# Performance work log

Measured on AMD Instinct MI355X. Metric: run time of the kernel, lower is better.

The kernel has to match this reference:

```python
import jax, jax.numpy as jnp
import numpy as np

DIM_IN = 1024
DIM_OUT = 1024


def setup_inputs() -> dict:
    key = jax.random.key(0)
    k1, k2, k3, k4 = jax.random.split(key, 4)
    X = jax.random.normal(k1, (4, 2048, DIM_IN), dtype=jnp.float32)
    s = 1.0 / np.sqrt(DIM_IN)
    Wq = jax.random.normal(k2, (DIM_IN, DIM_OUT), dtype=jnp.float32) * s
    Wk = jax.random.normal(k3, (DIM_IN, DIM_OUT), dtype=jnp.float32) * s
    Wv = jax.random.normal(k4, (DIM_IN, DIM_OUT), dtype=jnp.float32) * s
    return {"X": X, "Wq": Wq, "Wk": Wk, "Wv": Wv}


def reference(X, Wq, Wk, Wv):
    # X: [B, T, Din]; projections (qkv_bias=False)
    q = jnp.einsum('btd,de->bte', X, Wq)   # [B, T, Dout]
    k = jnp.einsum('btd,de->bte', X, Wk)
    v = jnp.einsum('btd,de->bte', X, Wv)
    T = X.shape[1]
    scores = jnp.einsum('bqe,bke->bqk', q, k)  # [B, T, T]
    causal = jnp.tril(jnp.ones((T, T), dtype=bool))  # mask upper triangle (future)
    scores = jnp.where(causal, scores, -jnp.inf)
    # scale=True: divide by sqrt(d); -inf stays -inf so order vs mask is irrelevant
    scores = scores / jnp.sqrt(jnp.asarray(k.shape[-1], dtype=scores.dtype))
    weights = jax.nn.softmax(scores, axis=-1)
    # dropout p=0.0 -> identity
    return jnp.einsum('bqk,bke->bqe', weights, v)
```

## Files before the change

kernel.cpp:

```cpp
#include <hip/hip_runtime.h>
#include <hip/hip_bf16.h>

typedef unsigned short u16;
typedef __bf16 bf16x8 __attribute__((ext_vector_type(8)));
typedef float f32x4 __attribute__((ext_vector_type(4)));
typedef unsigned short u16x8 __attribute__((ext_vector_type(8)));
typedef unsigned short u16x4 __attribute__((ext_vector_type(4)));

__device__ __forceinline__ float bf2f(u16 u) {
  unsigned int x = ((unsigned int)u) << 16;
  return __builtin_bit_cast(float, x);
}
__device__ __forceinline__ u16 f2bf(float f) {
  unsigned int x = __builtin_bit_cast(unsigned int, f);
  x = x + 0x7FFFu + ((x >> 16) & 1u);
  return (u16)(x >> 16);
}

__device__ __forceinline__ void gload_lds16(const u16* g, u16* l) {
  __builtin_amdgcn_global_load_lds(
      (const __attribute__((address_space(1))) unsigned int*)(unsigned long long)(uintptr_t)g,
      (__attribute__((address_space(3))) unsigned int*)(unsigned int)(uintptr_t)l,
      16, 0, 0);
}

__global__ __launch_bounds__(256) void prep_kernel(const float* __restrict__ X,
                                                   const float* __restrict__ Wq,
                                                   const float* __restrict__ Wk,
                                                   const float* __restrict__ Wv,
                                                   u16* __restrict__ Xb,
                                                   u16* __restrict__ Wt) {
  const int id = blockIdx.x;
  const int tid = threadIdx.x;
  if (id < 4096) {
    long i = ((long)id * 256 + tid) * 8;
    float4 a = *reinterpret_cast<const float4*>(X + i);
    float4 b = *reinterpret_cast<const float4*>(X + i + 4);
    u16x8 o;
    o[0] = f2bf(a.x); o[1] = f2bf(a.y); o[2] = f2bf(a.z); o[3] = f2bf(a.w);
    o[4] = f2bf(b.x); o[5] = f2bf(b.y); o[6] = f2bf(b.z); o[7] = f2bf(b.w);
    *reinterpret_cast<u16x8*>(Xb + i) = o;
    return;
  }
  __shared__ u16 t[64][72];
  const int id2 = id - 4096;
  const int z = id2 >> 8;
  const float* W = (z == 0) ? Wq : (z == 1) ? Wk : Wv;
  const float scale = (z == 0) ? (1.0f / 32.0f) : 1.0f;
  u16* out = Wt + (long)z * 1048576;
  const int c0 = (id2 & 15) * 64;
  const int r0 = ((id2 >> 4) & 15) * 64;
#pragma unroll
  for (int i = 0; i < 4; ++i) {
    int slot = tid + 256 * i;
    int lr = slot >> 4;
    int lc4 = slot & 15;
    float4 v = *reinterpret_cast<const float4*>(W + (long)(r0 + lr) * 1024 + c0 + lc4 * 4);
    t[lr][lc4 * 4 + 0] = f2bf(v.x * scale);
    t[lr][lc4 * 4 + 1] = f2bf(v.y * scale);
    t[lr][lc4 * 4 + 2] = f2bf(v.z * scale);
    t[lr][lc4 * 4 + 3] = f2bf(v.w * scale);
  }
  __syncthreads();
#pragma unroll
  for (int i = 0; i < 2; ++i) {
    int slot = tid + 256 * i;
    int orow = slot >> 3;
    int oc = slot & 7;
    u16x8 o;
#pragma unroll
    for (int j = 0; j < 8; ++j) o[j] = t[oc * 8 + j][orow];
    *reinterpret_cast<u16x8*>(out + (long)(c0 + orow) * 1024 + r0 + oc * 8) = o;
  }
}

__global__ __launch_bounds__(512, 4) void gemm_qkv(const u16* __restrict__ Xb,
                                                   const u16* __restrict__ Wt,
                                                   u16* __restrict__ Qb,
                                                   u16* __restrict__ Vt) {
  const int id = blockIdx.x;
  const int xcd = id & 7, j = id >> 3;
  const int bn = (xcd & 1) * 8 + (j & 7);
  const int bm = ((xcd >> 1) << 4) + (j >> 3);
  const int m0 = bm * 128, n0 = bn * 192;
  const int K = 1024;

  __shared__ u16 ldsA[2][8192];
  __shared__ u16 ldsB[2][12288];

  const int tid = threadIdx.x;
  const int lane = tid & 63;
  const int wid = tid >> 6;
  const int wm = wid >> 2, wn = wid & 3;
  const int l16 = lane & 15, lh = lane >> 4;
  const int strow = tid >> 3;
  const int scol = ((tid & 7) ^ (strow & 7)) * 8;
  const int rsw = l16 & 7;

  f32x4 acc[4][3];
#pragma unroll
  for (int mi = 0; mi < 4; ++mi)
#pragma unroll
    for (int ni = 0; ni < 3; ++ni) acc[mi][ni] = (f32x4)(0.0f);

  auto stage = [&](int d, int k0) {
#pragma unroll
    for (int l = 0; l < 2; ++l)
      gload_lds16(Xb + (long)(m0 + l * 64 + strow) * K + k0 + scol,
                  &ldsA[d][l * 4096 + tid * 8]);
#pragma unroll
    for (int l = 0; l < 3; ++l)
      gload_lds16(Wt + (long)(n0 + l * 64 + strow) * K + k0 + scol,
                  &ldsB[d][l * 4096 + tid * 8]);
  };

  stage(0, 0);
  int cur = 0;
  for (int k0 = 0; k0 < K; k0 += 64) {
    __syncthreads();
    if (k0 + 64 < K) stage(cur ^ 1, k0 + 64);
#pragma unroll
    for (int kk = 0; kk < 2; ++kk) {
      bf16x8 af[4], bfr[3];
#pragma unroll
      for (int mi = 0; mi < 4; ++mi)
        af[mi] = *reinterpret_cast<const bf16x8*>(
            &ldsA[cur][(wm * 64 + mi * 16 + l16) * 64 + (((kk * 4 + lh) ^ rsw)) * 8]);
#pragma unroll
      for (int ni = 0; ni < 3; ++ni)
        bfr[ni] = *reinterpret_cast<const bf16x8*>(
            &ldsB[cur][(wn * 48 + ni * 16 + l16) * 64 + (((kk * 4 + lh) ^ rsw)) * 8]);
#pragma unroll
      for (int mi = 0; mi < 4; ++mi)
#pragma unroll
        for (int ni = 0; ni < 3; ++ni)
          acc[mi][ni] = __builtin_amdgcn_mfma_f32_16x16x32_bf16(bfr[ni], af[mi], acc[mi][ni], 0, 0, 0);
    }
    cur ^= 1;
  }

  const int rowt = m0 + wm * 64 + l16;
#pragma unroll
  for (int ni = 0; ni < 3; ++ni) {
    const int gc0 = n0 + wn * 48 + ni * 16 + lh * 4;
    const int z = gc0 >> 10;
    const int lc = gc0 & 1023;
    if (z < 2) {
      u16* C = Qb + (long)z * 8388608;
#pragma unroll
      for (int mi = 0; mi < 4; ++mi) {
        u16x4 o;
#pragma unroll
        for (int r = 0; r < 4; ++r) o[r] = f2bf(acc[mi][ni][r]);
        *reinterpret_cast<u16x4*>(&C[(long)(rowt + mi * 16) * 1024 + lc]) = o;
      }
    } else {
#pragma unroll
      for (int mi = 0; mi < 4; ++mi) {
        const int grow = rowt + mi * 16;
        const int b = grow >> 11, t = grow & 2047;
#pragma unroll
        for (int r = 0; r < 4; ++r)
          Vt[(long)b * 2097152 + (long)(lc + r) * 2048 + t] = f2bf(acc[mi][ni][r]);
      }
    }
  }
}

__global__ __launch_bounds__(256, 3) void gemm_s(const u16* __restrict__ Qb,
                                                 const u16* __restrict__ Kb,
                                                 u16* __restrict__ Sg,
                                                 float* __restrict__ Sums) {
  const int id = blockIdx.y * 16 + blockIdx.x;
  const int xcd = id & 7, j = id >> 3;
  const int bn = j & 15;
  const int bm = (j >> 4) ? (15 - xcd) : xcd;
  const int bz = blockIdx.z;
  if (bn > bm) return;
  const int K = 1024;

  const u16* A = Qb + (long)bz * 2097152;
  const u16* B = Kb + (long)bz * 2097152;
  const int m0 = bm * 128, n0 = bn * 128;

  __shared__ u16 ldsA[2][4096];
  __shared__ u16 ldsB[2][4096];

  const int tid = threadIdx.x;
  const int lane = tid & 63;
  const int wid = tid >> 6;
  const int wm = wid >> 1, wn = wid & 1;
  const int l16 = lane & 15, lh = lane >> 4;
  const int strow = tid >> 2;
  const int scol = ((tid & 3) ^ ((strow >> 1) & 3)) * 8;

  f32x4 acc[4][4];
#pragma unroll
  for (int mi = 0; mi < 4; ++mi)
#pragma unroll
    for (int ni = 0; ni < 4; ++ni) acc[mi][ni] = (f32x4)(0.0f);

  auto stage = [&](int d, int k0) {
#pragma unroll
    for (int l = 0; l < 2; ++l) {
      const int row = l * 64 + strow;
      gload_lds16(A + (long)(m0 + row) * K + k0 + scol, &ldsA[d][l * 2048 + tid * 8]);
      gload_lds16(B + (long)(n0 + row) * K + k0 + scol, &ldsB[d][l * 2048 + tid * 8]);
    }
  };

  stage(0, 0);
  int cur = 0;
  for (int k0 = 0; k0 < K; k0 += 32) {
    __syncthreads();
    if (k0 + 32 < K) stage(cur ^ 1, k0 + 32);
    bf16x8 af[4], bfr[4];
#pragma unroll
    for (int mi = 0; mi < 4; ++mi) {
      const int row = wm * 64 + mi * 16 + l16;
      const int slot = lh ^ ((row >> 1) & 3);
      af[mi] = *reinterpret_cast<const bf16x8*>(&ldsA[cur][row * 32 + slot * 8]);
    }
#pragma unroll
    for (int ni = 0; ni < 4; ++ni) {
      const int row = wn * 64 + ni * 16 + l16;
      const int slot = lh ^ ((row >> 1) & 3);
      bfr[ni] = *reinterpret_cast<const bf16x8*>(&ldsB[cur][row * 32 + slot * 8]);
    }
#pragma unroll
    for (int mi = 0; mi < 4; ++mi)
#pragma unroll
      for (int ni = 0; ni < 4; ++ni)
        acc[mi][ni] = __builtin_amdgcn_mfma_f32_16x16x32_bf16(bfr[ni], af[mi], acc[mi][ni], 0, 0, 0);
    cur ^= 1;
  }

  u16* C = Sg + (long)bz * 4194304;
  float* sums = Sums + (long)bz * 2048;
  const long rown = (long)(m0 + wm * 64 + l16);
  const int coln = n0 + wn * 64 + lh * 4;
#pragma unroll
  for (int mi = 0; mi < 4; ++mi) {
    const int gr = m0 + wm * 64 + l16 + mi * 16;
    float rs = 0.0f;
#pragma unroll
    for (int ni = 0; ni < 4; ++ni) {
      u16x4 o;
#pragma unroll
      for (int r = 0; r < 4; ++r) {
        const int gc = coln + ni * 16 + r;
        const float e = (gc <= gr) ? __expf(acc[mi][ni][r]) : 0.0f;
        const u16 ub = f2bf(e);
        o[r] = ub;
        rs += bf2f(ub);
      }
      *reinterpret_cast<u16x4*>(&C[(rown + mi * 16) * 2048 + coln + ni * 16]) = o;
    }
    rs += __shfl_xor(rs, 16);
    rs += __shfl_xor(rs, 32);
    if (lh == 0) atomicAdd(&sums[gr], rs);
  }
}

__global__ __launch_bounds__(512, 2) void gemm_pv(const u16* __restrict__ Ag,
                                                  const u16* __restrict__ Bg,
                                                  float* __restrict__ Cg,
                                                  const float* __restrict__ Sums) {
  const int id = blockIdx.y * 8 + blockIdx.x;
  const int xcd = id & 7, j = id >> 3;
  const int bn = j & 7;
  const int bm = (j >> 3) ? (15 - xcd) : xcd;
  const int bz = blockIdx.z;
  const int K = 2048;

  const u16* A = Ag + (long)bz * 4194304;
  const u16* B = Bg + (long)bz * 2097152;
  const int m0 = bm * 128, n0 = bn * 128;
  const int kEnd = m0 + 128;

  __shared__ u16 ldsA[2][8192];
  __shared__ u16 ldsB[2][8192];

  const int tid = threadIdx.x;
  const int lane = tid & 63;
  const int wid = tid >> 6;
  const int wm = wid >> 2, wn = wid & 3;
  const int l16 = lane & 15, lh = lane >> 4;
  const int strow = tid >> 3;
  const int scol = ((tid & 7) ^ (strow & 7)) * 8;
  const int rsw = l16 & 7;

  f32x4 acc[4][2];
#pragma unroll
  for (int mi = 0; mi < 4; ++mi)
#pragma unroll
    for (int ni = 0; ni < 2; ++ni) acc[mi][ni] = (f32x4)(0.0f);

  auto stage = [&](int d, int k0) {
#pragma unroll
    for (int l = 0; l < 2; ++l) {
      const int row = l * 64 + strow;
      gload_lds16(A + (long)(m0 + row) * K + k0 + scol, &ldsA[d][l * 4096 + tid * 8]);
      gload_lds16(B + (long)(n0 + row) * K + k0 + scol, &ldsB[d][l * 4096 + tid * 8]);
    }
  };

  stage(0, 0);
  int cur = 0;
  for (int k0 = 0; k0 < kEnd; k0 += 64) {
    __syncthreads();
    if (k0 + 64 < kEnd) stage(cur ^ 1, k0 + 64);
#pragma unroll
    for (int kk = 0; kk < 2; ++kk) {
      bf16x8 af[4], bfr[2];
#pragma unroll
      for (int mi = 0; mi < 4; ++mi)
        af[mi] = *reinterpret_cast<const bf16x8*>(
            &ldsA[cur][(wm * 64 + mi * 16 + l16) * 64 + (((kk * 4 + lh) ^ rsw)) * 8]);
#pragma unroll
      for (int ni = 0; ni < 2; ++ni)
        bfr[ni] = *reinterpret_cast<const bf16x8*>(
            &ldsB[cur][(wn * 32 + ni * 16 + l16) * 64 + (((kk * 4 + lh) ^ rsw)) * 8]);
#pragma unroll
      for (int mi = 0; mi < 4; ++mi)
#pragma unroll
        for (int ni = 0; ni < 2; ++ni)
          acc[mi][ni] = __builtin_amdgcn_mfma_f32_16x16x32_bf16(bfr[ni], af[mi], acc[mi][ni], 0, 0, 0);
    }
    cur ^= 1;
  }

  float* C = Cg + (long)bz * 2097152;
  const float* sums = Sums + (long)bz * 2048;
  const long rown = (long)(m0 + wm * 64 + l16);
  const int coln = n0 + wn * 32 + lh * 4;
#pragma unroll
  for (int mi = 0; mi < 4; ++mi) {
    const float inv = 1.0f / sums[(int)rown + mi * 16];
#pragma unroll
    for (int ni = 0; ni < 2; ++ni) {
      f32x4 v = acc[mi][ni] * inv;
      *reinterpret_cast<f32x4*>(&C[(rown + mi * 16) * 1024 + coln + ni * 16]) = v;
    }
  }
}

extern "C" void kernel_launch(void* const* d_in, const int* in_sizes, int n_in,
                              void* d_out, int out_size, void* d_ws, size_t ws_size,
                              hipStream_t stream) {
  const float* X  = (const float*)d_in[0];
  const float* Wq = (const float*)d_in[1];
  const float* Wk = (const float*)d_in[2];
  const float* Wv = (const float*)d_in[3];

  u16* Xb = (u16*)d_ws;
  u16* Wt = Xb + 8388608;
  u16* Qb = Wt + 3145728;
  u16* Kb = Qb + 8388608;
  u16* Vt = Kb + 8388608;
  u16* S  = Vt + 8388608;
  float* sums = (float*)(S + 16777216);

  hipMemsetAsync(sums, 0, 4 * 2048 * sizeof(float), stream);

  prep_kernel<<<4864, 256, 0, stream>>>(X, Wq, Wk, Wv, Xb, Wt);

  gemm_qkv<<<1024, 512, 0, stream>>>(Xb, Wt, Qb, Vt);

  gemm_s<<<dim3(16, 16, 4), 256, 0, stream>>>(Qb, Kb, S, sums);

  gemm_pv<<<dim3(8, 16, 4), 512, 0, stream>>>(S, Vt, (float*)d_out, sums);
}
```

Measured before the change: 139.2 us.

## Launch only causal tiles in S GEMM with 64x128 tiles and XCD-balanced remap

The score GEMM grid becomes a flat 1D launch covering only the lower-triangular tiles (1088 blocks instead of 1024 with half returning early). It uses 64x128 tiles with a K-step of 64 and an 8-way XOR LDS swizzle, and block IDs are remapped so each XCD gets a balanced share of causal work. The PV GEMM also moves to a 1D grid whose remap assigns the N-tile by XCD and pairs light and heavy causal rows. This is meant to cut wasted empty blocks and even out load across XCDs, but smaller tiles lower per-block data reuse.

```diff
diff --git a/kernel.cpp b/kernel.cpp
--- a/kernel.cpp
+++ b/kernel.cpp
@@ -171,80 +171,83 @@
                                                  const u16* __restrict__ Kb,
                                                  u16* __restrict__ Sg,
                                                  float* __restrict__ Sums) {
-  const int id = blockIdx.y * 16 + blockIdx.x;
-  const int xcd = id & 7, j = id >> 3;
-  const int bn = j & 15;
-  const int bm = (j >> 4) ? (15 - xcd) : xcd;
-  const int bz = blockIdx.z;
-  if (bn > bm) return;
+  const int id = blockIdx.x;
+  const int x = id & 7;
+  const int q = id >> 3;
+  const int bz = q / 34;
+  int u = q - bz * 34;
+  int qr, kc;
+  const int n1 = 32 - 2 * x;
+  if (u < n1) { kc = x;      qr = 2 * x + u; }
+  else        { kc = 15 - x; qr = 30 - 2 * x + (u - n1); }
+  const int m0 = qr * 64, n0 = kc * 128;
   const int K = 1024;
 
   const u16* A = Qb + (long)bz * 2097152;
   const u16* B = Kb + (long)bz * 2097152;
-  const int m0 = bm * 128, n0 = bn * 128;
 
   __shared__ u16 ldsA[2][4096];
-  __shared__ u16 ldsB[2][4096];
+  __shared__ u16 ldsB[2][8192];
 
   const int tid = threadIdx.x;
   const int lane = tid & 63;
-  const int wid = tid >> 6;
-  const int wm = wid >> 1, wn = wid & 1;
+  const int wn = tid >> 6;
   const int l16 = lane & 15, lh = lane >> 4;
-  const int strow = tid >> 2;
-  const int scol = ((tid & 3) ^ ((strow >> 1) & 3)) * 8;
-
-  f32x4 acc[4][4];
+  const int strow = tid >> 3;
+  const int scol = ((tid & 7) ^ (strow & 7)) * 8;
+  const int rsw = l16 & 7;
+
+  f32x4 acc[4][2];
 #pragma unroll
   for (int mi = 0; mi < 4; ++mi)
 #pragma unroll
-    for (int ni = 0; ni < 4; ++ni) acc[mi][ni] = (f32x4)(0.0f);
+    for (int ni = 0; ni < 2; ++ni) acc[mi][ni] = (f32x4)(0.0f);
 
   auto stage = [&](int d, int k0) {
 #pragma unroll
-    for (int l = 0; l < 2; ++l) {
-      const int row = l * 64 + strow;
-      gload_lds16(A + (long)(m0 + row) * K + k0 + scol, &ldsA[d][l * 2048 + tid * 8]);
-      gload_lds16(B + (long)(n0 + row) * K + k0 + scol, &ldsB[d][l * 2048 + tid * 8]);
-    }
+    for (int l = 0; l < 2; ++l)
+      gload_lds16(A + (long)(m0 + l * 32 + strow) * K + k0 + scol,
+                  &ldsA[d][l * 2048 + tid * 8]);
+#pragma unroll
+    for (int l = 0; l < 4; ++l)
+      gload_lds16(B + (long)(n0 + l * 32 + strow) * K + k0 + scol,
+                  &ldsB[d][l * 2048 + tid * 8]);
   };
 
   stage(0, 0);
   int cur = 0;
-  for (int k0 = 0; k0 < K; k0 += 32) {
+  for (int k0 = 0; k0 < K; k0 += 64) {
     __syncthreads();
-    if (k0 + 32 < K) stage(cur ^ 1, k0 + 32);
-    bf16x8 af[4], bfr[4];
-#pragma unroll
-    for (int mi = 0; mi < 4; ++mi) {
-      const int row = wm * 64 + mi * 16 + l16;
-      const int slot = lh ^ ((row >> 1) & 3);
-      af[mi] = *reinterpret_cast<const bf16x8*>(&ldsA[cur][row * 32 + slot * 8]);
-    }
-#pragma unroll
-    for (int ni = 0; ni < 4; ++ni) {
-      const int row = wn * 64 + ni * 16 + l16;
-      const int slot = lh ^ ((row >> 1) & 3);
-      bfr[ni] = *reinterpret_cast<const bf16x8*>(&ldsB[cur][row * 32 + slot * 8]);
-    }
-#pragma unroll
-    for (int mi = 0; mi < 4; ++mi)
-#pragma unroll
-      for (int ni = 0; ni < 4; ++ni)
-        acc[mi][ni] = __builtin_amdgcn_mfma_f32_16x16x32_bf16(bfr[ni], af[mi], acc[mi][ni], 0, 0, 0);
+    if (k0 + 64 < K) stage(cur ^ 1, k0 + 64);
+#pragma unroll
+    for (int kk = 0; kk < 2; ++kk) {
+      bf16x8 af[4], bfr[2];
+#pragma unroll
+      for (int mi = 0; mi < 4; ++mi)
+        af[mi] = *reinterpret_cast<const bf16x8*>(
+            &ldsA[cur][(mi * 16 + l16) * 64 + (((kk * 4 + lh) ^ rsw)) * 8]);
+#pragma unroll
+      for (int ni = 0; ni < 2; ++ni)
+        bfr[ni] = *reinterpret_cast<const bf16x8*>(
+            &ldsB[cur][(wn * 32 + ni * 16 + l16) * 64 + (((kk * 4 + lh) ^ rsw)) * 8]);
+#pragma unroll
+      for (int mi = 0; mi < 4; ++mi)
+#pragma unroll
+        for (int ni = 0; ni < 2; ++ni)
+          acc[mi][ni] = __builtin_amdgcn_mfma_f32_16x16x32_bf16(bfr[ni], af[mi], acc[mi][ni], 0, 0, 0);
+    }
     cur ^= 1;
   }
 
   u16* C = Sg + (long)bz * 4194304;
   float* sums = Sums + (long)bz * 2048;
-  const long rown = (long)(m0 + wm * 64 + l16);
-  const int coln = n0 + wn * 64 + lh * 4;
+  const int coln = n0 + wn * 32 + lh * 4;
 #pragma unroll
   for (int mi = 0; mi < 4; ++mi) {
-    const int gr = m0 + wm * 64 + l16 + mi * 16;
+    const int gr = m0 + mi * 16 + l16;
     float rs = 0.0f;
 #pragma unroll
-    for (int ni = 0; ni < 4; ++ni) {
+    for (int ni = 0; ni < 2; ++ni) {
       u16x4 o;
 #pragma unroll
       for (int r = 0; r < 4; ++r) {
@@ -254,7 +257,7 @@
         o[r] = ub;
         rs += bf2f(ub);
       }
-      *reinterpret_cast<u16x4*>(&C[(rown + mi * 16) * 2048 + coln + ni * 16]) = o;
+      *reinterpret_cast<u16x4*>(&C[(long)gr * 2048 + coln + ni * 16]) = o;
     }
     rs += __shfl_xor(rs, 16);
     rs += __shfl_xor(rs, 32);
@@ -266,11 +269,15 @@
                                                   const u16* __restrict__ Bg,
                                                   float* __restrict__ Cg,
                                                   const float* __restrict__ Sums) {
-  const int id = blockIdx.y * 8 + blockIdx.x;
-  const int xcd = id & 7, j = id >> 3;
-  const int bn = j & 7;
-  const int bm = (j >> 3) ? (15 - xcd) : xcd;
-  const int bz = blockIdx.z;
+  const int id = blockIdx.x;
+  const int x = id & 7;
+  const int q = id >> 3;
+  const int f = (q ^ (q >> 5)) & 1;
+  const int i5 = ((q >> 1) & 15) | (((q >> 5) & 1) << 4);
+  const int bmb = i5 & 7;
+  const int bz = (i5 >> 3) & 3;
+  const int bm = f ? (15 - bmb) : bmb;
+  const int bn = x;
   const int K = 2048;
 
   const u16* A = Ag + (long)bz * 4194304;
@@ -367,7 +374,7 @@
 
   gemm_qkv<<<1024, 512, 0, stream>>>(Xb, Wt, Qb, Vt);
 
-  gemm_s<<<dim3(16, 16, 4), 256, 0, stream>>>(Qb, Kb, S, sums);
-
-  gemm_pv<<<dim3(8, 16, 4), 512, 0, stream>>>(S, Vt, (float*)d_out, sums);
-}
+  gemm_s<<<1088, 256, 0, stream>>>(Qb, Kb, S, sums);
+
+  gemm_pv<<<512, 512, 0, stream>>>(S, Vt, (float*)d_out, sums);
+}
```

Measured after the change: 132.3 us. 5.0% less time.
